# Performance work log

Measured on AMD Instinct MI355X. Metric: run time of the kernel, lower is better.

## Reference

```python
import jax, jax.numpy as jnp
import numpy as np

B, S, D_IN, D_OUT, RANK = 4, 2048, 4096, 4096, 32
BLOCK = 16
Q_MAX = 7.0  # INT4: 2**(4-1) - 1


def quantize_uniform(x, block_size=BLOCK, q_max=Q_MAX):
    """Block-wise symmetric fake-quantize (round-to-nearest, clamp)."""
    orig_shape = x.shape
    xf = x.reshape(-1, block_size)
    amax = jnp.clip(jnp.max(jnp.abs(xf), axis=-1, keepdims=True), 1e-12, None)
    scale = amax / q_max
    xq = jnp.clip(jnp.round(xf / scale), -q_max, q_max) * scale
    return xq.reshape(orig_shape)


def setup_inputs() -> dict:
    key = jax.random.key(0)
    ks = jax.random.split(key, 7)
    x = jax.random.normal(ks[0], (B, S, D_IN), jnp.float32)
    smooth_scale = jax.random.uniform(ks[1], (D_IN,), jnp.float32, 0.5, 2.0)
    w_quantized = jax.random.normal(ks[2], (D_OUT, D_IN), jnp.float32) * 0.02
    lora_a = jax.random.normal(ks[3], (RANK, D_IN), jnp.float32) * 0.02
    lora_b = jax.random.normal(ks[4], (D_OUT, RANK), jnp.float32) * 0.02
    w_sparse = jax.random.normal(ks[5], (D_OUT, D_IN), jnp.float32) * 0.02
    bias = jax.random.normal(ks[6], (D_OUT,), jnp.float32) * 0.02
    return {"x": x, "smooth_scale": smooth_scale, "w_quantized": w_quantized,
            "lora_a": lora_a, "lora_b": lora_b, "w_sparse": w_sparse, "bias": bias}


def reference(x, smooth_scale, w_quantized, lora_a, lora_b, w_sparse, bias):
    # smoothing (SmoothQuant-style per-channel scale)
    x_smoothed = x * smooth_scale                      # [B,S,Din]
    # block-wise INT4 fake-quantize of the smoothed activations
    x_q = quantize_uniform(x_smoothed)                 # [B,S,Din]
    # quantized main path
    base_out = jnp.einsum('bsi,oi->bso', x_q, w_quantized)
    # low-rank SVD error-correction path
    svd_out = jnp.einsum('bsr,or->bso',
                         jnp.einsum('bsi,ri->bsr', x_smoothed, lora_a),
                         lora_b)
    # sparse-outlier path (unsmoothed x)
    sparse_out = jnp.einsum('bsi,oi->bso', x, w_sparse)
    return base_out + svd_out + sparse_out + bias
```

## Files before the change

### kernel.cpp

```cpp
#include <hip/hip_runtime.h>
#include <stdint.h>

typedef float  f32x4  __attribute__((ext_vector_type(4)));
typedef __bf16 bf16x8 __attribute__((ext_vector_type(8)));
typedef unsigned int   u32;
typedef unsigned short u16;
typedef unsigned long long u64;
typedef u32 u32x4 __attribute__((ext_vector_type(4)));

#define M_TOT 8192
#define N_TOT 4096
#define K_DIN 4096
#define RANK  32
#define KCAT  8320
#define NTILE 130
#define KLAST 8256

__device__ __forceinline__ u16 f2bf(float f) {
  union { float f; u32 u; } v; v.f = f;
  u32 r = v.u + 0x7fffu + ((v.u >> 16) & 1u);
  return (u16)(r >> 16);
}

__global__ void prep_b_k(const float* __restrict__ wq, const float* __restrict__ wsp,
                         const float* __restrict__ lb, const float* __restrict__ la,
                         const float* __restrict__ ss,
                         u16* __restrict__ Bb, u16* __restrict__ asb) {
  const int b = blockIdx.x;
  const int tid = threadIdx.x;
  if (b < 32768) {
    const float* src = (b < 16384) ? wq : wsp;
    const int colofs = (b < 16384) ? 0 : K_DIN;
    const int i = (b & 16383) * 256 + tid;
    f32x4 v = ((const f32x4*)src)[i];
    int r = i >> 10, c = (i & 1023) * 4;
    alignas(8) u16 o[4] = { f2bf(v[0]), f2bf(v[1]), f2bf(v[2]), f2bf(v[3]) };
    *(u64*)(Bb + (size_t)r * KCAT + colofs + c) = *(const u64*)o;
  } else if (b < 32896) {
    const int i = (b - 32768) * 256 + tid;
    f32x4 v = ((const f32x4*)lb)[i];
    int row = i >> 3, c = (i & 7) * 4;
    alignas(8) u16 o[4] = { f2bf(v[0]), f2bf(v[1]), f2bf(v[2]), f2bf(v[3]) };
    u16* rp = Bb + (size_t)row * KCAT;
    *(u64*)(rp + 2 * K_DIN + c) = *(const u64*)o;
    u16* zp = rp + 2 * K_DIN + RANK + (i & 7) * 12;
    *(u64*)(zp + 0) = 0; *(u64*)(zp + 4) = 0; *(u64*)(zp + 8) = 0;
  } else {
    const int i = (b - 32896) * 256 + tid;
    f32x4 v = ((const f32x4*)la)[i];
    f32x4 s = ((const f32x4*)ss)[i & 1023];
    f32x4 p = v * s;
    alignas(8) u16 o[4] = { f2bf(p[0]), f2bf(p[1]), f2bf(p[2]), f2bf(p[3]) };
    *(u64*)(asb + 4 * (size_t)i) = *(const u64*)o;
  }
}

__global__ void prep_x_k(const float* __restrict__ x, const float* __restrict__ ss,
                         u16* __restrict__ Ab) {
  int m = blockIdx.x;
  int t = threadIdx.x;
  const f32x4* xp = (const f32x4*)(x + (size_t)m * K_DIN + t * 16);
  const f32x4* sp = (const f32x4*)(ss + t * 16);
  float xs[16];
  alignas(16) u16 rb[16], qb[16];
  float amax = 0.0f;
  #pragma unroll
  for (int i = 0; i < 4; ++i) {
    f32x4 a = xp[i], s = sp[i];
    #pragma unroll
    for (int j = 0; j < 4; ++j) {
      float xr = a[j];
      float v  = xr * s[j];
      xs[i*4+j] = v;
      amax = fmaxf(amax, fabsf(v));
      rb[i*4+j] = f2bf(xr);
    }
  }
  amax = fmaxf(amax, 1e-12f);
  float scale = amax / 7.0f;
  #pragma unroll
  for (int i = 0; i < 16; ++i) {
    float r = rintf(xs[i] / scale);
    r = fminf(7.0f, fmaxf(-7.0f, r));
    qb[i] = f2bf(r * scale);
  }
  u16* qo = Ab + (size_t)m * KCAT + t * 16;
  ((u32x4*)qo)[0] = ((const u32x4*)qb)[0];
  ((u32x4*)qo)[1] = ((const u32x4*)qb)[1];
  u16* ro = qo + K_DIN;
  ((u32x4*)ro)[0] = ((const u32x4*)rb)[0];
  ((u32x4*)ro)[1] = ((const u32x4*)rb)[1];
}

__global__ __launch_bounds__(256)
void lora_t_mfma_k(u16* __restrict__ Ab, const u16* __restrict__ asb) {
  const int wave = threadIdx.x >> 6;
  const int lane = threadIdx.x & 63;
  const int lr = lane & 15, lg = lane >> 4;
  const int m0 = blockIdx.x * 64 + wave * 16;
  f32x4 acc0 = {}, acc1 = {};
  for (int k0 = 0; k0 < K_DIN; k0 += 32) {
    bf16x8 a  = *(const bf16x8*)(Ab + (size_t)(m0 + lr) * KCAT + K_DIN + k0 + lg * 8);
    bf16x8 b0 = *(const bf16x8*)(asb + (size_t)lr        * K_DIN + k0 + lg * 8);
    bf16x8 b1 = *(const bf16x8*)(asb + (size_t)(16 + lr) * K_DIN + k0 + lg * 8);
    acc0 = __builtin_amdgcn_mfma_f32_16x16x32_bf16(a, b0, acc0, 0, 0, 0);
    acc1 = __builtin_amdgcn_mfma_f32_16x16x32_bf16(a, b1, acc1, 0, 0, 0);
  }
  #pragma unroll
  for (int j = 0; j < 4; ++j) {
    const int row = m0 + lg * 4 + j;
    Ab[(size_t)row * KCAT + 2 * K_DIN + lr]      = f2bf(acc0[j]);
    Ab[(size_t)row * KCAT + 2 * K_DIN + 16 + lr] = f2bf(acc1[j]);
  }
  const int zr = blockIdx.x * 64 + (threadIdx.x >> 2);
  u16* zp = Ab + (size_t)zr * KCAT + 2 * K_DIN + RANK + (threadIdx.x & 3) * 24;
  #pragma unroll
  for (int q = 0; q < 6; ++q) *(u64*)(zp + q * 4) = 0;
}

__device__ __forceinline__ void gld_lds16(const u16* g, u16* l) {
  __builtin_amdgcn_global_load_lds((const __attribute__((address_space(1))) u32*)g,
                                   (__attribute__((address_space(3))) u32*)l,
                                   16, 0, 0);
}

#define BAR()  __builtin_amdgcn_s_barrier()
#define VMW6() asm volatile("s_waitcnt vmcnt(6)" ::: "memory")
#define BUF1 32768

#define LDA(bufel, mh) do { _Pragma("unroll")                                        \
  for (int m_ = 0; m_ < 4; ++m_) {                                                   \
    Ar[m_][0] = *(const bf16x8*)(smem + (bufel) + aoff + ((mh)*4+m_)*1024 + blk0);    \
    Ar[m_][1] = *(const bf16x8*)(smem + (bufel) + aoff + ((mh)*4+m_)*1024 + blk1);    \
  } } while (0)

#define LDB(bufel, nh) do { _Pragma("unroll")                                        \
  for (int n_ = 0; n_ < 2; ++n_) {                                                   \
    Br[(nh)*2+n_][0] = *(const bf16x8*)(smem + (bufel) + boff + ((nh)*2+n_)*1024 + blk0); \
    Br[(nh)*2+n_][1] = *(const bf16x8*)(smem + (bufel) + boff + ((nh)*2+n_)*1024 + blk1); \
  } } while (0)

#define MMQ(mh, nh) do {                                                             \
  __builtin_amdgcn_s_setprio(1);                                                     \
  _Pragma("unroll")                                                                  \
  for (int m_ = 0; m_ < 4; ++m_) { _Pragma("unroll")                                 \
    for (int n_ = 0; n_ < 2; ++n_) {                                                 \
      acc[(mh)*4+m_][(nh)*2+n_] = __builtin_amdgcn_mfma_f32_16x16x32_bf16(           \
          Ar[m_][0], Br[(nh)*2+n_][0], acc[(mh)*4+m_][(nh)*2+n_], 0, 0, 0);          \
      acc[(mh)*4+m_][(nh)*2+n_] = __builtin_amdgcn_mfma_f32_16x16x32_bf16(           \
          Ar[m_][1], Br[(nh)*2+n_][1], acc[(mh)*4+m_][(nh)*2+n_], 0, 0, 0);          \
    } }                                                                              \
  __builtin_amdgcn_s_setprio(0);                                                     \
} while (0)

__global__ __launch_bounds__(512, 2)
void gemm8_k(const u16* __restrict__ Ab, const u16* __restrict__ Bb,
             const float* __restrict__ bias, float* __restrict__ out) {
  extern __shared__ u16 smem[];
  const int tid  = threadIdx.x;
  const int wave = tid >> 6;
  const int lane = tid & 63;
  const int lr = lane & 15, lg = lane >> 4;
  const int wm = wave >> 2, wn = wave & 3;

  const int wg  = blockIdx.x;
  const int swz = (wg & 7) * 64 + (wg >> 3);
  const int m0 = (swz >> 4) * 256;
  const int n0 = (swz & 15) * 256;

  const int aoff = wm * 8192 + lr * 64;
  const int boff = 16384 + wn * 4096 + lr * 64;
  const int e7   = lr & 7;
  const int blk0 = ((0 + lg) ^ e7) * 8;
  const int blk1 = ((4 + lg) ^ e7) * 8;

  const int srow = tid >> 3;
  const int scol = ((tid & 7) ^ (srow & 7)) * 8;
  const int woff = wave * 512;

  const u16* aRow = Ab + (size_t)(m0 + srow) * KCAT + scol;
  const u16* bRow = Bb + (size_t)(n0 + srow) * KCAT + scol;
  u16* dstA0 = smem + woff;
  u16* dstB0 = smem + 16384 + woff;

  bf16x8 Ar[4][2], Br[4][2];
  f32x4 acc[8][4] = {};

  auto stgA = [&](int kof, int h, int bufel) {
    u16* dst = dstA0 + bufel + h * 8192;
    gld_lds16(aRow + (size_t)(h * 128) * KCAT + kof, dst);
    gld_lds16(aRow + (size_t)(h * 128 + 64) * KCAT + kof, dst + 4096);
  };
  auto stgB = [&](int kof, int h, int bufel) {
    u16* dst = dstB0 + bufel + h * 8192;
    gld_lds16(bRow + (size_t)(h * 128) * KCAT + kof, dst);
    gld_lds16(bRow + (size_t)(h * 128 + 64) * KCAT + kof, dst + 4096);
  };

  stgA(0, 0, 0);     stgA(0, 1, 0);
  stgB(0, 0, 0);     stgB(0, 1, 0);
  stgB(64, 0, BUF1); stgB(64, 1, BUF1);
  stgA(64, 0, BUF1);
  VMW6();
  BAR();

  for (int it = 0; it < NTILE / 2; ++it) {
    const int ka = it * 128;
    int c2 = ka + 128, c3 = ka + 192;
    if (c2 > KLAST) c2 = KLAST;
    if (c3 > KLAST) c3 = KLAST;
    LDA(0, 0); LDB(0, 0);
    stgA(ka + 64, 1, BUF1);
    BAR(); MMQ(0, 0); BAR();
    LDB(0, 1);
    BAR(); MMQ(0, 1); BAR();
    LDA(0, 1);
    stgB(c2, 0, 0); stgB(c2, 1, 0);
    BAR(); MMQ(1, 1); BAR();
    stgA(c2, 0, 0);
    BAR(); MMQ(1, 0);
    VMW6();
    BAR();
    LDA(BUF1, 0); LDB(BUF1, 0);
    stgA(c2, 1, 0);
    BAR(); MMQ(0, 0); BAR();
    LDB(BUF1, 1);
    BAR(); MMQ(0, 1); BAR();
    LDA(BUF1, 1);
    stgB(c3, 0, BUF1); stgB(c3, 1, BUF1);
    BAR(); MMQ(1, 1); BAR();
    stgA(c3, 0, BUF1);
    BAR(); MMQ(1, 0);
    VMW6();
    BAR();
  }

  float bv[4];
  #pragma unroll
  for (int n = 0; n < 4; ++n) bv[n] = bias[n0 + wn * 64 + n * 16 + lr];
  #pragma unroll
  for (int m = 0; m < 8; ++m) {
    const int row = m0 + wm * 128 + m * 16 + lg * 4;
    #pragma unroll
    for (int n = 0; n < 4; ++n) {
      const int col = n0 + wn * 64 + n * 16 + lr;
      float* op = out + (size_t)row * N_TOT + col;
      op[0 * (size_t)N_TOT] = acc[m][n][0] + bv[n];
      op[1 * (size_t)N_TOT] = acc[m][n][1] + bv[n];
      op[2 * (size_t)N_TOT] = acc[m][n][2] + bv[n];
      op[3 * (size_t)N_TOT] = acc[m][n][3] + bv[n];
    }
  }
}

extern "C" void kernel_launch(void* const* d_in, const int* in_sizes, int n_in,
                              void* d_out, int out_size, void* d_ws, size_t ws_size,
                              hipStream_t stream) {
  const float* x    = (const float*)d_in[0];
  const float* ss   = (const float*)d_in[1];
  const float* wq   = (const float*)d_in[2];
  const float* la   = (const float*)d_in[3];
  const float* lb   = (const float*)d_in[4];
  const float* wsp  = (const float*)d_in[5];
  const float* bias = (const float*)d_in[6];
  float* out = (float*)d_out;

  uint8_t* w = (uint8_t*)d_ws;
  u16* Ab  = (u16*)w;  w += (size_t)M_TOT * KCAT * 2;
  u16* Bb  = (u16*)w;  w += (size_t)N_TOT * KCAT * 2;
  u16* asb = (u16*)w;

  prep_b_k<<<33024, 256, 0, stream>>>(wq, wsp, lb, la, ss, Bb, asb);
  prep_x_k<<<M_TOT, 256, 0, stream>>>(x, ss, Ab);
  lora_t_mfma_k<<<M_TOT / 64, 256, 0, stream>>>(Ab, asb);

  hipFuncSetAttribute((const void*)gemm8_k,
                      hipFuncAttributeMaxDynamicSharedMemorySize, 131072);
  gemm8_k<<<dim3((N_TOT / 256) * (M_TOT / 256)), 512, 131072, stream>>>(
      Ab, Bb, bias, out);
}
```

Before: 586.2 us.

## Fold smoothing and LoRA into combined weight, quantize via error term, drop barriers

The product is rewritten as x·(ss∘Wq + Wsp + B·(A∘ss))ᵀ + e·Wqᵀ, where e = x_q − x_smoothed is the quantization error. The prep kernels now build that merged weight and the bf16 error activations. This removes the separate LoRA MFMA kernel and the padded rank-32 K tail, so the GEMM K drops from 8320 to 8192. Several s_barrier calls around the MFMA phases of the main loop are also removed to reduce synchronisation stalls, which risks LDS read/write hazards between waves.

```diff
diff --git a/kernel.cpp b/kernel.cpp
--- a/kernel.cpp
+++ b/kernel.cpp
@@ -12,9 +12,9 @@
 #define N_TOT 4096
 #define K_DIN 4096
 #define RANK  32
-#define KCAT  8320
-#define NTILE 130
-#define KLAST 8256
+#define KCAT  8192
+#define NTILE 128
+#define KLAST 8128
 
 __device__ __forceinline__ u16 f2bf(float f) {
   union { float f; u32 u; } v; v.f = f;
@@ -22,37 +22,38 @@
   return (u16)(r >> 16);
 }
 
+__global__ void prep_ast_k(const float* __restrict__ la, const float* __restrict__ ss,
+                           float* __restrict__ asT) {
+  int idx = blockIdx.x * 256 + threadIdx.x;
+  int r = idx & 31, i = idx >> 5;
+  asT[(size_t)i * 32 + r] = la[(size_t)r * K_DIN + i] * ss[i];
+}
+
 __global__ void prep_b_k(const float* __restrict__ wq, const float* __restrict__ wsp,
-                         const float* __restrict__ lb, const float* __restrict__ la,
-                         const float* __restrict__ ss,
-                         u16* __restrict__ Bb, u16* __restrict__ asb) {
-  const int b = blockIdx.x;
-  const int tid = threadIdx.x;
-  if (b < 32768) {
-    const float* src = (b < 16384) ? wq : wsp;
-    const int colofs = (b < 16384) ? 0 : K_DIN;
-    const int i = (b & 16383) * 256 + tid;
-    f32x4 v = ((const f32x4*)src)[i];
-    int r = i >> 10, c = (i & 1023) * 4;
-    alignas(8) u16 o[4] = { f2bf(v[0]), f2bf(v[1]), f2bf(v[2]), f2bf(v[3]) };
-    *(u64*)(Bb + (size_t)r * KCAT + colofs + c) = *(const u64*)o;
-  } else if (b < 32896) {
-    const int i = (b - 32768) * 256 + tid;
-    f32x4 v = ((const f32x4*)lb)[i];
-    int row = i >> 3, c = (i & 7) * 4;
-    alignas(8) u16 o[4] = { f2bf(v[0]), f2bf(v[1]), f2bf(v[2]), f2bf(v[3]) };
-    u16* rp = Bb + (size_t)row * KCAT;
-    *(u64*)(rp + 2 * K_DIN + c) = *(const u64*)o;
-    u16* zp = rp + 2 * K_DIN + RANK + (i & 7) * 12;
-    *(u64*)(zp + 0) = 0; *(u64*)(zp + 4) = 0; *(u64*)(zp + 8) = 0;
-  } else {
-    const int i = (b - 32896) * 256 + tid;
-    f32x4 v = ((const f32x4*)la)[i];
-    f32x4 s = ((const f32x4*)ss)[i & 1023];
-    f32x4 p = v * s;
-    alignas(8) u16 o[4] = { f2bf(p[0]), f2bf(p[1]), f2bf(p[2]), f2bf(p[3]) };
-    *(u64*)(asb + 4 * (size_t)i) = *(const u64*)o;
-  }
+                         const float* __restrict__ lb, const float* __restrict__ asT,
+                         const float* __restrict__ ss, u16* __restrict__ Bb) {
+  int idx = blockIdx.x * 256 + threadIdx.x;
+  int o = idx >> 10, i = (idx & 1023) * 4;
+  f32x4 wqv = *(const f32x4*)(wq  + (size_t)o * K_DIN + i);
+  f32x4 wsv = *(const f32x4*)(wsp + (size_t)o * K_DIN + i);
+  f32x4 sv  = *(const f32x4*)(ss + i);
+  float acc[4];
+  #pragma unroll
+  for (int j = 0; j < 4; ++j) acc[j] = sv[j] * wqv[j] + wsv[j];
+  const f32x4* lbv = (const f32x4*)(lb + (size_t)o * RANK);
+  #pragma unroll
+  for (int q = 0; q < 8; ++q) {
+    f32x4 lv = lbv[q];
+    #pragma unroll
+    for (int j = 0; j < 4; ++j) {
+      f32x4 av = *(const f32x4*)(asT + (size_t)(i + j) * RANK + q * 4);
+      acc[j] += av[0]*lv[0] + av[1]*lv[1] + av[2]*lv[2] + av[3]*lv[3];
+    }
+  }
+  alignas(8) u16 o1[4] = { f2bf(acc[0]), f2bf(acc[1]), f2bf(acc[2]), f2bf(acc[3]) };
+  *(u64*)(Bb + (size_t)o * KCAT + i) = *(const u64*)o1;
+  alignas(8) u16 o2[4] = { f2bf(wqv[0]), f2bf(wqv[1]), f2bf(wqv[2]), f2bf(wqv[3]) };
+  *(u64*)(Bb + (size_t)o * KCAT + K_DIN + i) = *(const u64*)o2;
 }
 
 __global__ void prep_x_k(const float* __restrict__ x, const float* __restrict__ ss,
@@ -62,7 +63,7 @@
   const f32x4* xp = (const f32x4*)(x + (size_t)m * K_DIN + t * 16);
   const f32x4* sp = (const f32x4*)(ss + t * 16);
   float xs[16];
-  alignas(16) u16 rb[16], qb[16];
+  alignas(16) u16 rb[16], eb[16];
   float amax = 0.0f;
   #pragma unroll
   for (int i = 0; i < 4; ++i) {
@@ -82,40 +83,14 @@
   for (int i = 0; i < 16; ++i) {
     float r = rintf(xs[i] / scale);
     r = fminf(7.0f, fmaxf(-7.0f, r));
-    qb[i] = f2bf(r * scale);
-  }
-  u16* qo = Ab + (size_t)m * KCAT + t * 16;
-  ((u32x4*)qo)[0] = ((const u32x4*)qb)[0];
-  ((u32x4*)qo)[1] = ((const u32x4*)qb)[1];
-  u16* ro = qo + K_DIN;
+    eb[i] = f2bf(r * scale - xs[i]);
+  }
+  u16* ro = Ab + (size_t)m * KCAT + t * 16;
   ((u32x4*)ro)[0] = ((const u32x4*)rb)[0];
   ((u32x4*)ro)[1] = ((const u32x4*)rb)[1];
-}
-
-__global__ __launch_bounds__(256)
-void lora_t_mfma_k(u16* __restrict__ Ab, const u16* __restrict__ asb) {
-  const int wave = threadIdx.x >> 6;
-  const int lane = threadIdx.x & 63;
-  const int lr = lane & 15, lg = lane >> 4;
-  const int m0 = blockIdx.x * 64 + wave * 16;
-  f32x4 acc0 = {}, acc1 = {};
-  for (int k0 = 0; k0 < K_DIN; k0 += 32) {
-    bf16x8 a  = *(const bf16x8*)(Ab + (size_t)(m0 + lr) * KCAT + K_DIN + k0 + lg * 8);
-    bf16x8 b0 = *(const bf16x8*)(asb + (size_t)lr        * K_DIN + k0 + lg * 8);
-    bf16x8 b1 = *(const bf16x8*)(asb + (size_t)(16 + lr) * K_DIN + k0 + lg * 8);
-    acc0 = __builtin_amdgcn_mfma_f32_16x16x32_bf16(a, b0, acc0, 0, 0, 0);
-    acc1 = __builtin_amdgcn_mfma_f32_16x16x32_bf16(a, b1, acc1, 0, 0, 0);
-  }
-  #pragma unroll
-  for (int j = 0; j < 4; ++j) {
-    const int row = m0 + lg * 4 + j;
-    Ab[(size_t)row * KCAT + 2 * K_DIN + lr]      = f2bf(acc0[j]);
-    Ab[(size_t)row * KCAT + 2 * K_DIN + 16 + lr] = f2bf(acc1[j]);
-  }
-  const int zr = blockIdx.x * 64 + (threadIdx.x >> 2);
-  u16* zp = Ab + (size_t)zr * KCAT + 2 * K_DIN + RANK + (threadIdx.x & 3) * 24;
-  #pragma unroll
-  for (int q = 0; q < 6; ++q) *(u64*)(zp + q * 4) = 0;
+  u16* eo = ro + K_DIN;
+  ((u32x4*)eo)[0] = ((const u32x4*)eb)[0];
+  ((u32x4*)eo)[1] = ((const u32x4*)eb)[1];
 }
 
 __device__ __forceinline__ void gld_lds16(const u16* g, u16* l) {
@@ -211,26 +186,28 @@
     if (c3 > KLAST) c3 = KLAST;
     LDA(0, 0); LDB(0, 0);
     stgA(ka + 64, 1, BUF1);
-    BAR(); MMQ(0, 0); BAR();
+    MMQ(0, 0);
     LDB(0, 1);
-    BAR(); MMQ(0, 1); BAR();
+    MMQ(0, 1);
+    BAR();
     LDA(0, 1);
     stgB(c2, 0, 0); stgB(c2, 1, 0);
-    BAR(); MMQ(1, 1); BAR();
+    MMQ(1, 1);
     stgA(c2, 0, 0);
-    BAR(); MMQ(1, 0);
+    MMQ(1, 0);
     VMW6();
     BAR();
     LDA(BUF1, 0); LDB(BUF1, 0);
     stgA(c2, 1, 0);
-    BAR(); MMQ(0, 0); BAR();
+    MMQ(0, 0);
     LDB(BUF1, 1);
-    BAR(); MMQ(0, 1); BAR();
+    MMQ(0, 1);
+    BAR();
     LDA(BUF1, 1);
     stgB(c3, 0, BUF1); stgB(c3, 1, BUF1);
-    BAR(); MMQ(1, 1); BAR();
+    MMQ(1, 1);
     stgA(c3, 0, BUF1);
-    BAR(); MMQ(1, 0);
+    MMQ(1, 0);
     VMW6();
     BAR();
   }
@@ -266,13 +243,13 @@
   float* out = (float*)d_out;
 
   uint8_t* w = (uint8_t*)d_ws;
-  u16* Ab  = (u16*)w;  w += (size_t)M_TOT * KCAT * 2;
-  u16* Bb  = (u16*)w;  w += (size_t)N_TOT * KCAT * 2;
-  u16* asb = (u16*)w;
-
-  prep_b_k<<<33024, 256, 0, stream>>>(wq, wsp, lb, la, ss, Bb, asb);
+  u16* Ab   = (u16*)w;  w += (size_t)M_TOT * KCAT * 2;
+  u16* Bb   = (u16*)w;  w += (size_t)N_TOT * KCAT * 2;
+  float* asT = (float*)w;
+
+  prep_ast_k<<<512, 256, 0, stream>>>(la, ss, asT);
+  prep_b_k<<<16384, 256, 0, stream>>>(wq, wsp, lb, asT, ss, Bb);
   prep_x_k<<<M_TOT, 256, 0, stream>>>(x, ss, Ab);
-  lora_t_mfma_k<<<M_TOT / 64, 256, 0, stream>>>(Ab, asb);
 
   hipFuncSetAttribute((const void*)gemm8_k,
                       hipFuncAttributeMaxDynamicSharedMemorySize, 131072);
```

Measured after the change: 919.3 us. +56.8%, slower.
